# Performance work log

Hardware: AMD Instinct MI355X
Metric: run time of the kernel (lower is better)

## Reference

```python
import jax, jax.numpy as jnp
import numpy as np

B, T, W, L, H, TW = 4, 8192, 1024, 1024, 8, 4
D = L // H
A_SCALE = 8.0  # RG-LRU 'c' constant


def setup_inputs() -> dict:
    key = jax.random.key(0)
    ks = jax.random.split(key, 12)
    nrm = lambda k, shape, std: jax.random.normal(k, shape, jnp.float32) * std
    x = jax.random.normal(ks[0], (B, T, W), jnp.float32)
    segment_pos = jnp.tile(jnp.arange(T, dtype=jnp.int32)[None, :], (B, 1))
    Wy = nrm(ks[1], (W, L), (1.0 / W) ** 0.5)
    by = jnp.zeros((L,), jnp.float32)
    Wx = nrm(ks[2], (W, L), (1.0 / W) ** 0.5)
    bx = jnp.zeros((L,), jnp.float32)
    Wout = nrm(ks[3], (L, W), (1.0 / L) ** 0.5)
    bout = jnp.zeros((W,), jnp.float32)
    conv_w = nrm(ks[4], (TW, L), (1.0 / (TW * L)) ** 0.5)
    conv_b = jnp.zeros((L,), jnp.float32)
    # a_param init: radius in [0.9, 0.999], stored pre-softplus (Griffin rnn_param_init)
    u = jax.random.uniform(ks[5], (L,), jnp.float32)
    a_real = 0.5 * jnp.log(u * (0.999 ** 2 - 0.9 ** 2) + 0.9 ** 2 + 1e-8)  # negative
    a_param = jnp.log(jnp.expm1(-a_real))  # softplus(a_param) == -a_real
    igate_w = nrm(ks[6], (H, D, D), (1.0 / D) ** 0.5)
    igate_b = jnp.zeros((H, D), jnp.float32)
    agate_w = nrm(ks[7], (H, D, D), (1.0 / D) ** 0.5)
    agate_b = jnp.zeros((H, D), jnp.float32)
    return dict(x=x, segment_pos=segment_pos, Wy=Wy, by=by, Wx=Wx, bx=bx,
                conv_w=conv_w, conv_b=conv_b, a_param=a_param,
                igate_w=igate_w, igate_b=igate_b, agate_w=agate_w, agate_b=agate_b,
                Wout=Wout, bout=bout)


def _forward(x, segment_pos, Wy, by, Wx, bx, conv_w, conv_b, a_param,
             igate_w, igate_b, agate_w, agate_b, Wout, bout):
    pos = segment_pos  # [B, T]
    # gating branch
    y = jax.nn.gelu(x @ Wy + by, approximate=True)  # [B,T,L]
    # recurrent branch: linear_x -> causal depthwise conv1d -> RG-LRU
    u = x @ Wx + bx  # [B,T,L]
    acc = jnp.zeros_like(u)
    for i in range(TW):  # small fixed temporal width
        shift = TW - 1 - i
        u_sh = jnp.pad(u, ((0, 0), (shift, 0), (0, 0)))[:, :T]
        valid = (pos >= shift)[..., None]  # zero across segment boundaries
        acc = acc + jnp.where(valid, u_sh * conv_w[i], 0.0)
    u = acc + conv_b  # [B,T,L]
    # RG-LRU gates (block-diagonal per head)
    ur = u.reshape(B, T, H, D)
    gate_x = jax.nn.sigmoid(jnp.einsum('bthd,hde->bthe', ur, igate_w) + igate_b).reshape(B, T, L)
    gate_a = jax.nn.sigmoid(jnp.einsum('bthd,hde->bthe', ur, agate_w) + agate_b).reshape(B, T, L)
    log_a = -A_SCALE * gate_a * jax.nn.softplus(a_param)  # [B,T,L]
    a = jnp.exp(log_a)
    multiplier = jnp.sqrt(1.0 - jnp.exp(2.0 * log_a))
    reset = (pos == 0)[..., None]
    normed_x = (u * gate_x) * jnp.where(reset, 1.0, multiplier)
    a_m = jnp.where(reset, 0.0, a)
    # linear recurrence h_t = a_t * h_{t-1} + normed_x_t via associative scan
    def combine(c1, c2):
        a1, b1 = c1
        a2, b2 = c2
        return (a1 * a2, a2 * b1 + b2)
    _, h = jax.lax.associative_scan(combine, (a_m, normed_x), axis=1)
    return (h * y) @ Wout + bout  # [B,T,W]


def reference(x, segment_pos, Wy, by, Wx, bx, conv_w, conv_b, a_param,
              igate_w, igate_b, agate_w, agate_b, Wout, bout):
    return _forward(x, segment_pos, Wy, by, Wx, bx, conv_w, conv_b, a_param,
                    igate_w, igate_b, agate_w, agate_b, Wout, bout)
```

## Files before the change

### kernel.cpp

```cpp
#include <hip/hip_runtime.h>
#include <cstdint>
#include <cstddef>

#define B_ 4
#define T_ 8192
#define W_ 1024
#define L_ 1024
#define H_ 8
#define D_ 128
#define TW_ 4
#define BT_ (B_*T_)
#define CHUNK_ 32
#define NCH_ (T_/CHUNK_)

typedef __bf16 bf16_t;
typedef __bf16 bf16x8 __attribute__((ext_vector_type(8)));
typedef float  f32x4  __attribute__((ext_vector_type(4)));

__device__ __forceinline__ float  bf2f(bf16_t x){ return (float)x; }
__device__ __forceinline__ bf16_t f2bf(float x){ return (bf16_t)x; }

__device__ __forceinline__ float rcp_ (float x){ return __builtin_amdgcn_rcpf(x); }
__device__ __forceinline__ float sqrt_(float x){ return __builtin_amdgcn_sqrtf(x); }
__device__ __forceinline__ float exp2_(float x){ return __builtin_amdgcn_exp2f(x); }
__device__ __forceinline__ float log2_(float x){ return __builtin_amdgcn_logf(x); }
#define LOG2E_ 1.4426950408889634f

__device__ __forceinline__ float sigmoid_fast(float z){
  return rcp_(1.0f + exp2_(-LOG2E_*z));
}
__device__ __forceinline__ float softplus_fast(float x){
  return (x > 15.0f) ? x : 0.6931471805599453f * log2_(1.0f + exp2_(LOG2E_*x));
}
__device__ __forceinline__ float gelu_fast(float z){
  float g = 0.7978845608028654f*(z + 0.044715f*z*z*z);
  float e = exp2_(-2.8853900817779268f*fabsf(g));
  float th = (1.0f - e)*rcp_(1.0f + e);
  th = copysignf(th, g);
  return 0.5f*z*(1.0f + th);
}

__device__ __forceinline__ void stage16(const bf16_t* g, bf16_t* l){
  __builtin_amdgcn_global_load_lds((const __attribute__((address_space(1))) void*)g,
                                   (__attribute__((address_space(3))) void*)l, 16, 0, 0);
}
__device__ __forceinline__ void stage_tile(const bf16_t* __restrict__ gbase, int ldg,
                                           bf16_t* lds, int wave, int lane){
  #pragma unroll
  for (int c2 = 0; c2 < 2; ++c2){
    int chunk = wave*2 + c2;
    int row = chunk*16 + (lane >> 2);
    int col = (lane & 3)*8;
    stage16(gbase + (size_t)row*ldg + col, lds + chunk*512 + lane*8);
  }
}

__global__ void __launch_bounds__(256) cvt_kernel(const float* __restrict__ in,
                                                  bf16_t* __restrict__ out, int n8){
  int g = blockIdx.x*256 + threadIdx.x;
  if (g >= n8) return;
  f32x4 a = *(const f32x4*)(in + (size_t)g*8);
  f32x4 b = *(const f32x4*)(in + (size_t)g*8 + 4);
  bf16x8 o;
  #pragma unroll
  for (int e=0;e<4;e++){ o[e] = f2bf(a[e]); o[4+e] = f2bf(b[e]); }
  *(bf16x8*)(out + (size_t)g*8) = o;
}

__global__ void __launch_bounds__(256) transpose_f2b(const float* __restrict__ in,
                                                     bf16_t* __restrict__ out, int R, int C){
  __shared__ float tile[32][33];
  size_t mb = (size_t)blockIdx.z * R * C;
  int c0 = blockIdx.x*32, r0 = blockIdx.y*32;
  int tx = threadIdx.x, ty = threadIdx.y;
  #pragma unroll
  for (int i = ty; i < 32; i += 8)
    tile[i][tx] = in[mb + (size_t)(r0+i)*C + c0 + tx];
  __syncthreads();
  #pragma unroll
  for (int i = ty; i < 32; i += 8)
    out[mb + (size_t)(c0+i)*R + r0 + tx] = f2bf(tile[tx][i]);
}

__global__ void __launch_bounds__(256,2) gemm_xw_kernel(
    const bf16_t* __restrict__ X,
    const bf16_t* __restrict__ WyT, const bf16_t* __restrict__ WxT,
    const float* __restrict__ by,  const float* __restrict__ bx,
    bf16_t* __restrict__ Y, bf16_t* __restrict__ U0)
{
  __shared__ __align__(16) bf16_t As [128*32];
  __shared__ __align__(16) bf16_t Bys[128*32];
  __shared__ __align__(16) bf16_t Bxs[128*32];
  __shared__ __align__(16) bf16_t scr_g[4][1280];
  const int K = W_;
  int tid = threadIdx.x, wave = tid>>6, lane = tid&63;
  int wm = wave>>1, wn = wave&1, q = lane>>4, ml = lane&15;
  int lin = blockIdx.x;
  int nl = (lin & 7)*256 + (lin >> 3);
  int bm = nl >> 3, j = nl & 7;
  const bf16_t* Wyp = WyT + (size_t)j*128*K;
  const bf16_t* Wxp = WxT + (size_t)j*128*K;
  f32x4 accY[4][4] = {}, accX[4][4] = {};
  for (int k0 = 0; k0 < K; k0 += 32){
    stage_tile(X + (size_t)bm*128*K + k0, K, As, wave, lane);
    stage_tile(Wyp + k0, K, Bys, wave, lane);
    stage_tile(Wxp + k0, K, Bxs, wave, lane);
    __syncthreads();
    bf16x8 af[4], bvy[4], bvx[4];
    #pragma unroll
    for (int i=0;i<4;i++) af[i]  = *(const bf16x8*)(As  + (wm*64 + i*16 + ml)*32 + q*8);
    #pragma unroll
    for (int i=0;i<4;i++) bvy[i] = *(const bf16x8*)(Bys + (wn*64 + i*16 + ml)*32 + q*8);
    #pragma unroll
    for (int i=0;i<4;i++) bvx[i] = *(const bf16x8*)(Bxs + (wn*64 + i*16 + ml)*32 + q*8);
    #pragma unroll
    for (int i=0;i<4;i++)
      #pragma unroll
      for (int n=0;n<4;n++){
        accY[i][n] = __builtin_amdgcn_mfma_f32_16x16x32_bf16(af[i], bvy[n], accY[i][n], 0,0,0);
        accX[i][n] = __builtin_amdgcn_mfma_f32_16x16x32_bf16(af[i], bvx[n], accX[i][n], 0,0,0);
      }
    __syncthreads();
  }
  float bbY[4], bbX[4];
  #pragma unroll
  for (int n=0;n<4;n++){
    int col = j*128 + wn*64 + n*16 + ml;
    bbY[n] = by[col]; bbX[n] = bx[col];
  }
  bf16_t* s0 = scr_g[wave];
  bf16_t* s1 = s0 + 640;
  int rrow = lane>>2, cgp = lane&3;
  size_t mbase = (size_t)bm*128 + wm*64;
  #pragma unroll
  for (int i=0;i<4;i++){
    size_t grow = mbase + i*16 + rrow;
    int gc = j*128 + wn*64 + cgp*8;
    #pragma unroll
    for (int n=0;n<4;n++){
      bf16_t* sp = (n<2) ? s0 : s1;
      #pragma unroll
      for (int r=0;r<4;r++)
        sp[(q*4+r)*40 + (n&1)*16 + ml] = f2bf(gelu_fast(accY[i][n][r] + bbY[n]));
    }
    {
      bf16x8 v0 = *(const bf16x8*)(s0 + rrow*40 + cgp*8);
      bf16x8 v1 = *(const bf16x8*)(s1 + rrow*40 + cgp*8);
      *(bf16x8*)(Y + grow*L_ + gc)      = v0;
      *(bf16x8*)(Y + grow*L_ + gc + 32) = v1;
    }
    #pragma unroll
    for (int n=0;n<4;n++){
      bf16_t* sp = (n<2) ? s0 : s1;
      #pragma unroll
      for (int r=0;r<4;r++)
        sp[(q*4+r)*40 + (n&1)*16 + ml] = f2bf(accX[i][n][r] + bbX[n]);
    }
    {
      bf16x8 v0 = *(const bf16x8*)(s0 + rrow*40 + cgp*8);
      bf16x8 v1 = *(const bf16x8*)(s1 + rrow*40 + cgp*8);
      *(bf16x8*)(U0 + grow*L_ + gc)      = v0;
      *(bf16x8*)(U0 + grow*L_ + gc + 32) = v1;
    }
  }
}

__global__ void __launch_bounds__(256,2) gate_kernel(
    const bf16_t* __restrict__ U0,
    const bf16_t* __restrict__ igTw, const bf16_t* __restrict__ agTw,
    const float* __restrict__ igb,  const float* __restrict__ agb,
    const float* __restrict__ a_param,
    const float* __restrict__ conv_w, const float* __restrict__ conv_b,
    const int* __restrict__ segpos,
    bf16_t* __restrict__ XN, bf16_t* __restrict__ L2A)
{
  __shared__ __align__(16) bf16_t As[4*128*32];
  __shared__ __align__(16) bf16_t scr_g[4][2560];
  int tid = threadIdx.x, wave = tid>>6, lane = tid&63;
  int wm = wave>>1, wn = wave&1, q = lane>>4, ml = lane&15;
  int bm = blockIdx.x, h = blockIdx.y;

  {
    int cg = tid & 15, rg = tid >> 4;
    int col = cg*8;
    int kcc = col >> 5, c32 = col & 31;
    const bf16_t* up = U0 + ((size_t)bm*128 + (size_t)rg*8)*L_ + h*128 + col;
    f32x4 wta[4], wtb[4];
    #pragma unroll
    for (int s=0;s<4;s++){
      wta[s] = *(const f32x4*)(conv_w + (size_t)(3-s)*L_ + h*128 + col);
      wtb[s] = *(const f32x4*)(conv_w + (size_t)(3-s)*L_ + h*128 + col + 4);
    }
    f32x4 cba = *(const f32x4*)(conv_b + h*128 + col);
    f32x4 cbb = *(const f32x4*)(conv_b + h*128 + col + 4);
    bool first = (bm & 63) == 0;
    int r0 = rg*8;
    bf16x8 zero8 = {};
    bf16x8 m1 = (!first || r0 >= 1) ? *(const bf16x8*)(up - 1*L_) : zero8;
    bf16x8 m2 = (!first || r0 >= 2) ? *(const bf16x8*)(up - 2*L_) : zero8;
    bf16x8 m3 = (!first || r0 >= 3) ? *(const bf16x8*)(up - 3*L_) : zero8;
    #pragma unroll
    for (int r=0;r<8;r++){
      bf16x8 cur = *(const bf16x8*)(up + (size_t)r*L_);
      bf16x8 ov;
      #pragma unroll
      for (int e=0;e<4;e++){
        float v0 = cba[e] + bf2f(cur[e])*wta[0][e] + bf2f(m1[e])*wta[1][e]
                          + bf2f(m2[e])*wta[2][e] + bf2f(m3[e])*wta[3][e];
        float v1 = cbb[e] + bf2f(cur[4+e])*wtb[0][e] + bf2f(m1[4+e])*wtb[1][e]
                          + bf2f(m2[4+e])*wtb[2][e] + bf2f(m3[4+e])*wtb[3][e];
        ov[e] = f2bf(v0); ov[4+e] = f2bf(v1);
      }
      *(bf16x8*)(As + kcc*4096 + (size_t)(r0+r)*32 + c32) = ov;
      m3 = m2; m2 = m1; m1 = cur;
    }
  }
  __syncthreads();

  const bf16_t* igp = igTw + (size_t)h*D_*D_;
  const bf16_t* agp = agTw + (size_t)h*D_*D_;
  f32x4 ax[4][4] = {}, aa[4][4] = {};
  #pragma unroll
  for (int kc=0; kc<4; ++kc){
    bf16x8 af[4], bx_[4], ba_[4];
    #pragma unroll
    for (int i=0;i<4;i++) af[i]  = *(const bf16x8*)(As + kc*4096 + (wm*64 + i*16 + ml)*32 + q*8);
    #pragma unroll
    for (int n=0;n<4;n++) bx_[n] = *(const bf16x8*)(igp + (size_t)(wn*64 + n*16 + ml)*128 + kc*32 + q*8);
    #pragma unroll
    for (int n=0;n<4;n++) ba_[n] = *(const bf16x8*)(agp + (size_t)(wn*64 + n*16 + ml)*128 + kc*32 + q*8);
    #pragma unroll
    for (int i=0;i<4;i++)
      #pragma unroll
      for (int n=0;n<4;n++){
        ax[i][n] = __builtin_amdgcn_mfma_f32_16x16x32_bf16(af[i], bx_[n], ax[i][n], 0,0,0);
        aa[i][n] = __builtin_amdgcn_mfma_f32_16x16x32_bf16(af[i], ba_[n], aa[i][n], 0,0,0);
      }
  }

  bf16_t* sx0 = scr_g[wave];
  bf16_t* sx1 = sx0 + 640;
  bf16_t* sa0 = sx0 + 1280;
  bf16_t* sa1 = sx0 + 1920;
  int rrow = lane>>2, cgp = lane&3;
  size_t mbase = (size_t)bm*128 + wm*64;
  float bb_x[4], bb_a[4], spa4[4]; int kc4[4], ci4[4];
  #pragma unroll
  for (int n=0;n<4;n++){
    int e = wn*64 + n*16 + ml;
    int l = h*D_ + e;
    bb_x[n] = igb[l]; bb_a[n] = agb[l]; spa4[n] = softplus_fast(a_param[l]);
    kc4[n] = e>>5; ci4[n] = e&31;
  }
  #pragma unroll
  for (int i=0;i<4;i++){
    #pragma unroll
    for (int r=0;r<4;r++){
      int rl = wm*64 + i*16 + q*4 + r;
      size_t row = mbase + i*16 + q*4 + r;
      bool reset = (segpos[row] == 0);
      #pragma unroll
      for (int n=0;n<4;n++){
        float uval = bf2f(As[kc4[n]*4096 + rl*32 + ci4[n]]);
        float gx = sigmoid_fast(ax[i][n][r] + bb_x[n]);
        float ga = sigmoid_fast(aa[i][n][r] + bb_a[n]);
        float l2a = -11.541560327111707f * ga * spa4[n];
        float mult = reset ? 1.0f : sqrt_(fmaxf(0.0f, 1.0f - exp2_(2.0f*l2a)));
        bf16_t xnv = f2bf(uval * gx * mult);
        bf16_t lav = f2bf(reset ? -1e30f : l2a);
        int so = (q*4+r)*40 + (n&1)*16 + ml;
        if (n < 2){ sx0[so] = xnv; sa0[so] = lav; }
        else      { sx1[so] = xnv; sa1[so] = lav; }
      }
    }
    size_t grow = mbase + i*16 + rrow;
    int gc = h*D_ + wn*64 + cgp*8;
    bf16x8 xv0 = *(const bf16x8*)(sx0 + rrow*40 + cgp*8);
    bf16x8 xv1 = *(const bf16x8*)(sx1 + rrow*40 + cgp*8);
    *(bf16x8*)(XN + grow*L_ + gc)      = xv0;
    *(bf16x8*)(XN + grow*L_ + gc + 32) = xv1;
    bf16x8 av0 = *(const bf16x8*)(sa0 + rrow*40 + cgp*8);
    bf16x8 av1 = *(const bf16x8*)(sa1 + rrow*40 + cgp*8);
    *(bf16x8*)(L2A + grow*L_ + gc)      = av0;
    *(bf16x8*)(L2A + grow*L_ + gc + 32) = av1;
  }
}

__global__ void __launch_bounds__(128) scan1_kernel(const bf16_t* __restrict__ L2A,
    const bf16_t* __restrict__ XN, float* __restrict__ Aarr, float* __restrict__ Barr)
{
  int lg = threadIdx.x;
  int c = blockIdx.y, b = blockIdx.z;
  int l = lg*8;
  size_t base = ((size_t)b*T_ + (size_t)c*CHUNK_)*L_ + l;
  float suml[8] = {}, brun[8] = {};
  #pragma unroll 4
  for (int t = 0; t < CHUNK_; ++t){
    bf16x8 la = *(const bf16x8*)(L2A + base + (size_t)t*L_);
    bf16x8 xv = *(const bf16x8*)(XN  + base + (size_t)t*L_);
    #pragma unroll
    for (int e=0;e<8;e++){
      float lf = bf2f(la[e]);
      suml[e] += lf;
      brun[e] = exp2_(lf)*brun[e] + bf2f(xv[e]);
    }
  }
  size_t ci = ((size_t)b*NCH_ + c)*L_ + l;
  f32x4 a0, a1, b0, b1;
  #pragma unroll
  for (int e=0;e<4;e++){
    a0[e] = exp2_(suml[e]);   a1[e] = exp2_(suml[4+e]);
    b0[e] = brun[e];          b1[e] = brun[4+e];
  }
  *(f32x4*)(Aarr + ci)     = a0;  *(f32x4*)(Aarr + ci + 4) = a1;
  *(f32x4*)(Barr + ci)     = b0;  *(f32x4*)(Barr + ci + 4) = b1;
}

__global__ void __launch_bounds__(256) scan2_kernel(const float* __restrict__ Aarr,
    const float* __restrict__ Barr, float* __restrict__ Carr)
{
  int l4 = threadIdx.x;
  int b = blockIdx.y;
  f32x4 h = {0.f, 0.f, 0.f, 0.f};
  for (int c = 0; c < NCH_; ++c){
    size_t ci = ((size_t)b*NCH_ + c)*L_ + (size_t)l4*4;
    f32x4 a  = *(const f32x4*)(Aarr + ci);
    f32x4 bb = *(const f32x4*)(Barr + ci);
    *(f32x4*)(Carr + ci) = h;
    #pragma unroll
    for (int e=0;e<4;e++) h[e] = a[e]*h[e] + bb[e];
  }
}

__global__ void __launch_bounds__(128) scan3_kernel(const bf16_t* __restrict__ L2A,
    const bf16_t* __restrict__ XN, const bf16_t* __restrict__ Y,
    const float* __restrict__ Carr, bf16_t* __restrict__ HY)
{
  int lg = threadIdx.x;
  int c = blockIdx.y, b = blockIdx.z;
  int l = lg*8;
  size_t base = ((size_t)b*T_ + (size_t)c*CHUNK_)*L_ + l;
  size_t ci = ((size_t)b*NCH_ + c)*L_ + l;
  f32x4 h0 = *(const f32x4*)(Carr + ci);
  f32x4 h1 = *(const f32x4*)(Carr + ci + 4);
  float h[8];
  #pragma unroll
  for (int e=0;e<4;e++){ h[e] = h0[e]; h[4+e] = h1[e]; }
  #pragma unroll 4
  for (int t = 0; t < CHUNK_; ++t){
    bf16x8 la = *(const bf16x8*)(L2A + base + (size_t)t*L_);
    bf16x8 xv = *(const bf16x8*)(XN  + base + (size_t)t*L_);
    bf16x8 yv = *(const bf16x8*)(Y   + base + (size_t)t*L_);
    bf16x8 o;
    #pragma unroll
    for (int e=0;e<8;e++){
      h[e] = exp2_(bf2f(la[e]))*h[e] + bf2f(xv[e]);
      o[e] = f2bf(h[e]*bf2f(yv[e]));
    }
    *(bf16x8*)(HY + base + (size_t)t*L_) = o;
  }
}

__global__ void __launch_bounds__(256,2) gemm_out_kernel(
    const bf16_t* __restrict__ A_, const bf16_t* __restrict__ WoT,
    const float* __restrict__ bo, float* __restrict__ Out)
{
  __shared__ __align__(16) bf16_t As[128*32];
  __shared__ __align__(16) bf16_t Bs[128*32];
  __shared__ __align__(16) char scr_[4][1280];
  const int K = L_;
  int tid = threadIdx.x, wave = tid>>6, lane = tid&63;
  int wm = wave>>1, wn = wave&1, q = lane>>4, ml = lane&15;
  int lin = blockIdx.x;
  int nl = (lin & 7)*256 + (lin >> 3);
  int bm = nl >> 3, j = nl & 7;
  const bf16_t* Bp = WoT + (size_t)j*128*K;
  f32x4 acc[4][4] = {};
  for (int k0 = 0; k0 < K; k0 += 32){
    stage_tile(A_ + (size_t)bm*128*K + k0, K, As, wave, lane);
    stage_tile(Bp + k0, K, Bs, wave, lane);
    __syncthreads();
    bf16x8 af[4], bv[4];
    #pragma unroll
    for (int i=0;i<4;i++) af[i] = *(const bf16x8*)(As + (wm*64 + i*16 + ml)*32 + q*8);
    #pragma unroll
    for (int i=0;i<4;i++) bv[i] = *(const bf16x8*)(Bs + (wn*64 + i*16 + ml)*32 + q*8);
    #pragma unroll
    for (int i=0;i<4;i++)
      #pragma unroll
      for (int n=0;n<4;n++)
        acc[i][n] = __builtin_amdgcn_mfma_f32_16x16x32_bf16(af[i], bv[n], acc[i][n], 0,0,0);
    __syncthreads();
  }
  float bb[4];
  #pragma unroll
  for (int n=0;n<4;n++) bb[n] = bo[j*128 + wn*64 + n*16 + ml];
  float* scrf = (float*)scr_[wave];
  int rrow = lane>>2, cgp = lane&3;
  size_t mbase = (size_t)bm*128 + wm*64;
  #pragma unroll
  for (int i=0;i<4;i++){
    size_t grow = mbase + i*16 + rrow;
    #pragma unroll
    for (int n=0;n<4;n++){
      #pragma unroll
      for (int r=0;r<4;r++) scrf[(q*4+r)*20 + ml] = acc[i][n][r] + bb[n];
      f32x4 ov = *(const f32x4*)(scrf + rrow*20 + cgp*4);
      *(f32x4*)(Out + grow*W_ + j*128 + wn*64 + n*16 + cgp*4) = ov;
    }
  }
}

extern "C" void kernel_launch(void* const* d_in, const int* in_sizes, int n_in,
                              void* d_out, int out_size, void* d_ws, size_t ws_size,
                              hipStream_t stream)
{
  (void)in_sizes; (void)n_in; (void)out_size;
  const float* x      = (const float*)d_in[0];
  const int*   segpos = (const int*)  d_in[1];
  const float* Wy     = (const float*)d_in[2];
  const float* by     = (const float*)d_in[3];
  const float* Wx     = (const float*)d_in[4];
  const float* bx     = (const float*)d_in[5];
  const float* conv_w = (const float*)d_in[6];
  const float* conv_b = (const float*)d_in[7];
  const float* a_par  = (const float*)d_in[8];
  const float* igw    = (const float*)d_in[9];
  const float* igb    = (const float*)d_in[10];
  const float* agw    = (const float*)d_in[11];
  const float* agb    = (const float*)d_in[12];
  const float* Wout   = (const float*)d_in[13];
  const float* bout   = (const float*)d_in[14];
  float* out = (float*)d_out;

  char* ws = (char*)d_ws;
  size_t off = 0;
  auto alloc = [&](size_t bytes)->void*{ void* p = ws + off; off += (bytes + 255) & ~(size_t)255; return p; };
  bf16_t* Xbf  = (bf16_t*)alloc((size_t)BT_*W_*2);
  bf16_t* WyT  = (bf16_t*)alloc((size_t)W_*L_*2);
  bf16_t* WxT  = (bf16_t*)alloc((size_t)W_*L_*2);
  bf16_t* WoT  = (bf16_t*)alloc((size_t)L_*W_*2);
  bf16_t* igTw = (bf16_t*)alloc((size_t)H_*D_*D_*2);
  bf16_t* agTw = (bf16_t*)alloc((size_t)H_*D_*D_*2);
  bf16_t* Y    = (bf16_t*)alloc((size_t)BT_*L_*2);
  bf16_t* U0   = (bf16_t*)alloc((size_t)BT_*L_*2);
  bf16_t* XN   = (bf16_t*)alloc((size_t)BT_*L_*2);
  float*  Aarr = (float*) alloc((size_t)B_*NCH_*L_*4);
  float*  Barr = (float*) alloc((size_t)B_*NCH_*L_*4);
  float*  Carr = (float*) alloc((size_t)B_*NCH_*L_*4);
  if (ws_size < off) return;

  bf16_t* L2A = Xbf;
  bf16_t* HY  = U0;

  cvt_kernel<<<dim3(BT_*W_/8/256), 256, 0, stream>>>(x, Xbf, BT_*W_/8);

  dim3 tb(32, 8);
  transpose_f2b<<<dim3(32,32,1), tb, 0, stream>>>(Wy,   WyT, 1024, 1024);
  transpose_f2b<<<dim3(32,32,1), tb, 0, stream>>>(Wx,   WxT, 1024, 1024);
  transpose_f2b<<<dim3(32,32,1), tb, 0, stream>>>(Wout, WoT, 1024, 1024);
  transpose_f2b<<<dim3(4,4,H_),  tb, 0, stream>>>(igw,  igTw, 128, 128);
  transpose_f2b<<<dim3(4,4,H_),  tb, 0, stream>>>(agw,  agTw, 128, 128);

  gemm_xw_kernel<<<dim3(2048), 256, 0, stream>>>(Xbf, WyT, WxT, by, bx, Y, U0);
  gate_kernel<<<dim3(BT_/128, H_), 256, 0, stream>>>(U0, igTw, agTw, igb, agb, a_par,
                                                     conv_w, conv_b, segpos, XN, L2A);
  scan1_kernel<<<dim3(1, NCH_, B_), 128, 0, stream>>>(L2A, XN, Aarr, Barr);
  scan2_kernel<<<dim3(1, B_), 256, 0, stream>>>(Aarr, Barr, Carr);
  scan3_kernel<<<dim3(1, NCH_, B_), 128, 0, stream>>>(L2A, XN, Y, Carr, HY);
  gemm_out_kernel<<<dim3(2048), 256, 0, stream>>>(HY, WoT, bout, out);
}
```

Measured before the change: 705.0 us.

## Fuse chunk-local scan reduction into gate kernel and widen chunk to 64

The first pass of the chunked scan (per-chunk decay product and partial state) now happens inside the gate kernel's epilogue. It uses register running sums plus cross-lane shuffles over each wave's 64 rows, so the separate scan1 kernel that re-read L2A and XN from global memory is removed. The chunk size doubles to 64 to match the wave tile, which halves the number of chunks the serial scan2 walks. scan2 is split across more blocks, and scan3 uses 4-wide elements with 256 threads to keep parallelism with the longer chunks. The trade is extra exp2 and shuffle work in the gate kernel and a longer serial loop per thread in scan3.

```diff
diff --git a/kernel.cpp b/kernel.cpp
--- a/kernel.cpp
+++ b/kernel.cpp
@@ -10,11 +10,12 @@
 #define D_ 128
 #define TW_ 4
 #define BT_ (B_*T_)
-#define CHUNK_ 32
+#define CHUNK_ 64
 #define NCH_ (T_/CHUNK_)
 
 typedef __bf16 bf16_t;
 typedef __bf16 bf16x8 __attribute__((ext_vector_type(8)));
+typedef __bf16 bf16x4 __attribute__((ext_vector_type(4)));
 typedef float  f32x4  __attribute__((ext_vector_type(4)));
 
 __device__ __forceinline__ float  bf2f(bf16_t x){ return (float)x; }
@@ -172,7 +173,8 @@
     const float* __restrict__ a_param,
     const float* __restrict__ conv_w, const float* __restrict__ conv_b,
     const int* __restrict__ segpos,
-    bf16_t* __restrict__ XN, bf16_t* __restrict__ L2A)
+    bf16_t* __restrict__ XN, bf16_t* __restrict__ L2A,
+    float* __restrict__ Aarr, float* __restrict__ Barr)
 {
   __shared__ __align__(16) bf16_t As[4*128*32];
   __shared__ __align__(16) bf16_t scr_g[4][2560];
@@ -252,6 +254,7 @@
     bb_x[n] = igb[l]; bb_a[n] = agb[l]; spa4[n] = softplus_fast(a_param[l]);
     kc4[n] = e>>5; ci4[n] = e&31;
   }
+  float runS[4][4], runB[4][4];
   #pragma unroll
   for (int i=0;i<4;i++){
     #pragma unroll
@@ -271,6 +274,9 @@
         int so = (q*4+r)*40 + (n&1)*16 + ml;
         if (n < 2){ sx0[so] = xnv; sa0[so] = lav; }
         else      { sx1[so] = xnv; sa1[so] = lav; }
+        float lf = bf2f(lav), xf = bf2f(xnv);
+        if (r == 0){ runS[i][n] = lf;  runB[i][n] = xf; }
+        else       { runS[i][n] += lf; runB[i][n] = exp2_(lf)*runB[i][n] + xf; }
       }
     }
     size_t grow = mbase + i*16 + rrow;
@@ -284,44 +290,43 @@
     *(bf16x8*)(L2A + grow*L_ + gc)      = av0;
     *(bf16x8*)(L2A + grow*L_ + gc + 32) = av1;
   }
-}
-
-__global__ void __launch_bounds__(128) scan1_kernel(const bf16_t* __restrict__ L2A,
-    const bf16_t* __restrict__ XN, float* __restrict__ Aarr, float* __restrict__ Barr)
-{
-  int lg = threadIdx.x;
-  int c = blockIdx.y, b = blockIdx.z;
-  int l = lg*8;
-  size_t base = ((size_t)b*T_ + (size_t)c*CHUNK_)*L_ + l;
-  float suml[8] = {}, brun[8] = {};
-  #pragma unroll 4
-  for (int t = 0; t < CHUNK_; ++t){
-    bf16x8 la = *(const bf16x8*)(L2A + base + (size_t)t*L_);
-    bf16x8 xv = *(const bf16x8*)(XN  + base + (size_t)t*L_);
-    #pragma unroll
-    for (int e=0;e<8;e++){
-      float lf = bf2f(la[e]);
-      suml[e] += lf;
-      brun[e] = exp2_(lf)*brun[e] + bf2f(xv[e]);
-    }
-  }
-  size_t ci = ((size_t)b*NCH_ + c)*L_ + l;
-  f32x4 a0, a1, b0, b1;
-  #pragma unroll
-  for (int e=0;e<4;e++){
-    a0[e] = exp2_(suml[e]);   a1[e] = exp2_(suml[4+e]);
-    b0[e] = brun[e];          b1[e] = brun[4+e];
-  }
-  *(f32x4*)(Aarr + ci)     = a0;  *(f32x4*)(Aarr + ci + 4) = a1;
-  *(f32x4*)(Barr + ci)     = b0;  *(f32x4*)(Barr + ci + 4) = b1;
-}
-
-__global__ void __launch_bounds__(256) scan2_kernel(const float* __restrict__ Aarr,
+
+  int u16 = lane & 16, u32b = lane & 32;
+  float totS[4], totB[4];
+  #pragma unroll
+  for (int n=0;n<4;n++){
+    #pragma unroll
+    for (int i=0;i<4;i++){
+      float s = runS[i][n], b = runB[i][n];
+      float s2 = __shfl_xor(s, 16), b2 = __shfl_xor(b, 16);
+      float b1 = u16 ? (exp2_(s)*b2 + b) : (exp2_(s2)*b + b2);
+      float s1 = s + s2;
+      float s3 = __shfl_xor(s1, 32), b3 = __shfl_xor(b1, 32);
+      float bb = u32b ? (exp2_(s1)*b3 + b1) : (exp2_(s3)*b1 + b3);
+      float ss = s1 + s3;
+      if (i == 0){ totS[n] = ss; totB[n] = bb; }
+      else { totB[n] = exp2_(ss)*totB[n] + bb; totS[n] += ss; }
+    }
+  }
+  if (lane < 16){
+    int bb_ = bm >> 6;
+    int cc_ = (bm & 63)*2 + wm;
+    size_t ci = ((size_t)bb_*NCH_ + cc_)*L_ + h*D_ + wn*64 + ml;
+    #pragma unroll
+    for (int n=0;n<4;n++){
+      Aarr[ci + n*16] = exp2_(totS[n]);
+      Barr[ci + n*16] = totB[n];
+    }
+  }
+}
+
+__global__ void __launch_bounds__(64) scan2_kernel(const float* __restrict__ Aarr,
     const float* __restrict__ Barr, float* __restrict__ Carr)
 {
-  int l4 = threadIdx.x;
+  int l4 = blockIdx.x*64 + threadIdx.x;
   int b = blockIdx.y;
   f32x4 h = {0.f, 0.f, 0.f, 0.f};
+  #pragma unroll 4
   for (int c = 0; c < NCH_; ++c){
     size_t ci = ((size_t)b*NCH_ + c)*L_ + (size_t)l4*4;
     f32x4 a  = *(const f32x4*)(Aarr + ci);
@@ -332,32 +337,30 @@
   }
 }
 
-__global__ void __launch_bounds__(128) scan3_kernel(const bf16_t* __restrict__ L2A,
+__global__ void __launch_bounds__(256) scan3_kernel(const bf16_t* __restrict__ L2A,
     const bf16_t* __restrict__ XN, const bf16_t* __restrict__ Y,
     const float* __restrict__ Carr, bf16_t* __restrict__ HY)
 {
-  int lg = threadIdx.x;
+  int l = threadIdx.x*4;
   int c = blockIdx.y, b = blockIdx.z;
-  int l = lg*8;
   size_t base = ((size_t)b*T_ + (size_t)c*CHUNK_)*L_ + l;
   size_t ci = ((size_t)b*NCH_ + c)*L_ + l;
-  f32x4 h0 = *(const f32x4*)(Carr + ci);
-  f32x4 h1 = *(const f32x4*)(Carr + ci + 4);
-  float h[8];
-  #pragma unroll
-  for (int e=0;e<4;e++){ h[e] = h0[e]; h[4+e] = h1[e]; }
+  f32x4 hv = *(const f32x4*)(Carr + ci);
+  float h[4];
+  #pragma unroll
+  for (int e=0;e<4;e++) h[e] = hv[e];
   #pragma unroll 4
   for (int t = 0; t < CHUNK_; ++t){
-    bf16x8 la = *(const bf16x8*)(L2A + base + (size_t)t*L_);
-    bf16x8 xv = *(const bf16x8*)(XN  + base + (size_t)t*L_);
-    bf16x8 yv = *(const bf16x8*)(Y   + base + (size_t)t*L_);
-    bf16x8 o;
-    #pragma unroll
-    for (int e=0;e<8;e++){
+    bf16x4 la = *(const bf16x4*)(L2A + base + (size_t)t*L_);
+    bf16x4 xv = *(const bf16x4*)(XN  + base + (size_t)t*L_);
+    bf16x4 yv = *(const bf16x4*)(Y   + base + (size_t)t*L_);
+    bf16x4 o;
+    #pragma unroll
+    for (int e=0;e<4;e++){
       h[e] = exp2_(bf2f(la[e]))*h[e] + bf2f(xv[e]);
       o[e] = f2bf(h[e]*bf2f(yv[e]));
     }
-    *(bf16x8*)(HY + base + (size_t)t*L_) = o;
+    *(bf16x4*)(HY + base + (size_t)t*L_) = o;
   }
 }
 
@@ -464,9 +467,9 @@
 
   gemm_xw_kernel<<<dim3(2048), 256, 0, stream>>>(Xbf, WyT, WxT, by, bx, Y, U0);
   gate_kernel<<<dim3(BT_/128, H_), 256, 0, stream>>>(U0, igTw, agTw, igb, agb, a_par,
-                                                     conv_w, conv_b, segpos, XN, L2A);
-  scan1_kernel<<<dim3(1, NCH_, B_), 128, 0, stream>>>(L2A, XN, Aarr, Barr);
-  scan2_kernel<<<dim3(1, B_), 256, 0, stream>>>(Aarr, Barr, Carr);
-  scan3_kernel<<<dim3(1, NCH_, B_), 128, 0, stream>>>(L2A, XN, Y, Carr, HY);
+                                                     conv_w, conv_b, segpos, XN, L2A,
+                                                     Aarr, Barr);
+  scan2_kernel<<<dim3(4, B_), 64, 0, stream>>>(Aarr, Barr, Carr);
+  scan3_kernel<<<dim3(1, NCH_, B_), 256, 0, stream>>>(L2A, XN, Y, Carr, HY);
   gemm_out_kernel<<<dim3(2048), 256, 0, stream>>>(HY, WoT, bout, out);
 }
```

Result: faster. 665.4 us (-5.6%).
